# Kernel optimization log

Hardware: AMD Instinct MI355X
Metric: run time of the kernel (lower is better)

Reference implementation:

```python
import jax, jax.numpy as jnp
import numpy as np

EPS = 1e-5


def _layer_norm(x, w, b):
    mu = jnp.mean(x, axis=-1, keepdims=True)
    var = jnp.mean(jnp.square(x - mu), axis=-1, keepdims=True)
    return (x - mu) * jax.lax.rsqrt(var + EPS) * w + b


def setup_inputs() -> dict:
    key = jax.random.key(0)
    ks = jax.random.split(key, 6)
    B, S, N, CM, CZ, H = 1, 512, 512, 64, 128, 8
    return {
        "m_si": jax.random.normal(ks[0], (B, S, N, CM), jnp.float32),
        "z_ij": jax.random.normal(ks[1], (B, S, S, CZ), jnp.float32),
        "ln_m_w": jnp.ones((CM,), jnp.float32),
        "ln_m_b": jnp.zeros((CM,), jnp.float32),
        "ln_z_w": jnp.ones((CZ,), jnp.float32),
        "ln_z_b": jnp.zeros((CZ,), jnp.float32),
        "W_v": jax.random.normal(ks[2], (CM, CM), jnp.float32) / np.sqrt(CM),
        "W_b": jax.random.normal(ks[3], (H, CZ), jnp.float32) / np.sqrt(CZ),
        "W_g": jax.random.normal(ks[4], (CM, CM), jnp.float32) / np.sqrt(CM),
        "W_out": jax.random.normal(ks[5], (CM, CM), jnp.float32) / np.sqrt(CM),
    }


def reference(m_si, z_ij, ln_m_w, ln_m_b, ln_z_w, ln_z_b, W_v, W_b, W_g, W_out):
    H = W_b.shape[0]
    *lead, S, N, CM = m_si.shape
    D = CM // H  # head_dim

    m = _layer_norm(m_si, ln_m_w, ln_m_b)  # (..., s, n, c_m)

    # Pair bias logits -> softmax over j (second sequence axis)
    b = _layer_norm(z_ij, ln_z_w, ln_z_b) @ W_b.T          # (..., i, j, h)
    w = jax.nn.softmax(b, axis=-2)                          # softmax over j

    v = (m @ W_v.T).reshape(*lead, S, N, H, D)              # (..., j, n, h, d)
    g = jax.nn.sigmoid(m @ W_g.T).reshape(*lead, S, N, H, D)

    o = jnp.einsum("...ijh,...jnhd->...inhd", w, v)         # pair-weighted avg
    out = (g * o).reshape(*lead, S, N, CM) @ W_out.T
    return out
```

## Files before the change

kernel.cpp:

```cpp
#include <hip/hip_runtime.h>

typedef __bf16 bf16x8 __attribute__((ext_vector_type(8)));
typedef float  f32x4  __attribute__((ext_vector_type(4)));
typedef unsigned short u16x8 __attribute__((ext_vector_type(8)));

__device__ __forceinline__ float b2f(unsigned short u) {
    unsigned int x = ((unsigned int)u) << 16;
    float f; __builtin_memcpy(&f, &x, 4); return f;
}
__device__ __forceinline__ unsigned short f2b(float f) {
    unsigned int x; __builtin_memcpy(&x, &f, 4);
    unsigned int r = (x + 0x7FFFu + ((x >> 16) & 1u)) >> 16;
    return (unsigned short)r;
}
__device__ __forceinline__ void async16(void* lds, const void* g) {
    __builtin_amdgcn_global_load_lds((const __attribute__((address_space(1))) void*)g,
                                     (__attribute__((address_space(3))) void*)lds, 16, 0, 0);
}

__global__ __launch_bounds__(256) void k0_wcvt(
    const float* __restrict__ Wv, const float* __restrict__ Wg, unsigned short* __restrict__ Wp)
{
    const int idx = blockIdx.x * 256 + threadIdx.x;
    const int cg = idx >> 10, col = (idx >> 3) & 127, u = idx & 7;
    const int k = cg * 8 + u;
    const float v = (col < 64) ? Wv[col * 64 + k] : Wg[(col - 64) * 64 + k];
    Wp[idx] = f2b(v);
}

__global__ __launch_bounds__(256) void k1_ln_vg(
    const float* __restrict__ m, const float* __restrict__ lnw, const float* __restrict__ lnb,
    const unsigned short* __restrict__ Wp,
    unsigned short* __restrict__ vT, unsigned short* __restrict__ gB)
{
    __shared__ __align__(16) unsigned short Wl[8192];
    __shared__ __align__(16) unsigned short mhb[2048];
    __shared__ float vstage[32][65];
    __shared__ float gstage[32][65];
    const int t = threadIdx.x, w = t >> 6, lane = t & 63;
    const int n = blockIdx.x, s0 = blockIdx.y * 32;

#pragma unroll
    for (int r = 0; r < 4; r++)
        async16(&Wl[(r * 256 + t) * 8], Wp + (size_t)(r * 256 + t) * 8);

    const int rl = t >> 3, cg = t & 7, c8 = cg * 8;
    {
        const int s = s0 + rl;
        const float* src = &m[((size_t)s * 512 + n) * 64 + c8];
        float4 x0 = *(const float4*)src;
        float4 x1 = *(const float4*)(src + 4);
        float sum = x0.x+x0.y+x0.z+x0.w + x1.x+x1.y+x1.z+x1.w;
        float sq  = x0.x*x0.x+x0.y*x0.y+x0.z*x0.z+x0.w*x0.w
                  + x1.x*x1.x+x1.y*x1.y+x1.z*x1.z+x1.w*x1.w;
#pragma unroll
        for (int msk = 4; msk; msk >>= 1) { sum += __shfl_xor(sum, msk); sq += __shfl_xor(sq, msk); }
        float mu  = sum * (1.f / 64.f);
        float var = sq * (1.f / 64.f) - mu * mu;
        float rs  = rsqrtf(var + 1e-5f);
        float4 lw0 = *(const float4*)&lnw[c8], lw1 = *(const float4*)&lnw[c8 + 4];
        float4 lb0 = *(const float4*)&lnb[c8], lb1 = *(const float4*)&lnb[c8 + 4];
        u16x8 hb;
        hb[0] = f2b((x0.x - mu) * rs * lw0.x + lb0.x);
        hb[1] = f2b((x0.y - mu) * rs * lw0.y + lb0.y);
        hb[2] = f2b((x0.z - mu) * rs * lw0.z + lb0.z);
        hb[3] = f2b((x0.w - mu) * rs * lw0.w + lb0.w);
        hb[4] = f2b((x1.x - mu) * rs * lw1.x + lb1.x);
        hb[5] = f2b((x1.y - mu) * rs * lw1.y + lb1.y);
        hb[6] = f2b((x1.z - mu) * rs * lw1.z + lb1.z);
        hb[7] = f2b((x1.w - mu) * rs * lw1.w + lb1.w);
        *(u16x8*)&mhb[(cg * 32 + rl) * 8] = hb;
    }
    __syncthreads();

    const int quad = lane >> 4, lq = lane & 15;
    const int colbase = w * 32;
    f32x4 zero = {0.f, 0.f, 0.f, 0.f};
    f32x4 acc[2][2] = {{zero, zero}, {zero, zero}};
    bf16x8 af[2][2], bfr[2][2];
#pragma unroll
    for (int kk = 0; kk < 2; kk++) {
        const int ch = kk * 4 + quad;
#pragma unroll
        for (int mi = 0; mi < 2; mi++)
            af[mi][kk] = *(const bf16x8*)&mhb[(ch * 32 + mi * 16 + lq) * 8];
#pragma unroll
        for (int ni = 0; ni < 2; ni++)
            bfr[ni][kk] = *(const bf16x8*)&Wl[(ch * 128 + colbase + ni * 16 + lq) * 8];
    }
#pragma unroll
    for (int mi = 0; mi < 2; mi++)
#pragma unroll
        for (int ni = 0; ni < 2; ni++)
#pragma unroll
            for (int kk = 0; kk < 2; kk++)
                acc[mi][ni] = __builtin_amdgcn_mfma_f32_16x16x32_bf16(af[mi][kk], bfr[ni][kk], acc[mi][ni], 0, 0, 0);

    if (w < 2) {
#pragma unroll
        for (int mi = 0; mi < 2; mi++)
#pragma unroll
            for (int ni = 0; ni < 2; ni++)
#pragma unroll
                for (int rr = 0; rr < 4; rr++)
                    vstage[mi * 16 + quad * 4 + rr][colbase + ni * 16 + lq] = acc[mi][ni][rr];
    } else {
#pragma unroll
        for (int mi = 0; mi < 2; mi++)
#pragma unroll
            for (int ni = 0; ni < 2; ni++)
#pragma unroll
                for (int rr = 0; rr < 4; rr++) {
                    float gg = 1.f / (1.f + __expf(-acc[mi][ni][rr]));
                    gstage[mi * 16 + quad * 4 + rr][colbase - 64 + ni * 16 + lq] = gg;
                }
    }
    __syncthreads();

    {
        const int h = t >> 5, d = (t >> 2) & 7, jc = t & 3;
        u16x8 pk;
#pragma unroll
        for (int u = 0; u < 8; u++) pk[u] = f2b(vstage[jc * 8 + u][h * 8 + d]);
        size_t off = (size_t)h * 2097152 + (size_t)(n * 8 + d) * 512 + (size_t)(s0 + jc * 8);
        *(u16x8*)(vT + off) = pk;
    }
    {
        u16x8 gk;
#pragma unroll
        for (int u = 0; u < 8; u++) gk[u] = f2b(gstage[rl][c8 + u]);
        *(u16x8*)(gB + ((size_t)(s0 + rl) * 512 + n) * 64 + c8) = gk;
    }
}

__global__ __launch_bounds__(256) void k2_ln_b(
    const float* __restrict__ z, const float* __restrict__ lnw, const float* __restrict__ lnb,
    const float* __restrict__ Wb, float* __restrict__ bL)
{
    __shared__ float swb[1024];
    __shared__ float sw[128], sb[128];
    const int t = threadIdx.x;
    const int gtid = blockIdx.x * 256 + t;
    const int row = gtid >> 2, qt = gtid & 3;

    const float* src = z + (size_t)row * 128;
    float4 x[8];
#pragma unroll
    for (int q = 0; q < 8; q++)
        x[q] = *(const float4*)&src[q * 16 + qt * 4];

    *(float4*)&swb[t * 4] = *(const float4*)&Wb[t * 4];
    if (t < 32)      *(float4*)&sw[t * 4] = *(const float4*)&lnw[t * 4];
    else if (t < 64) *(float4*)&sb[(t - 32) * 4] = *(const float4*)&lnb[(t - 32) * 4];
    __syncthreads();

    float sum = 0.f, sq = 0.f;
#pragma unroll
    for (int q = 0; q < 8; q++) {
        sum += x[q].x + x[q].y + x[q].z + x[q].w;
        sq  += x[q].x*x[q].x + x[q].y*x[q].y + x[q].z*x[q].z + x[q].w*x[q].w;
    }
    sum += __shfl_xor(sum, 1); sq += __shfl_xor(sq, 1);
    sum += __shfl_xor(sum, 2); sq += __shfl_xor(sq, 2);
    const float mu  = sum * (1.f / 128.f);
    const float var = sq * (1.f / 128.f) - mu * mu;
    const float rs  = rsqrtf(var + 1e-5f);

    float acc[8];
#pragma unroll
    for (int h = 0; h < 8; h++) acc[h] = 0.f;
#pragma unroll
    for (int q = 0; q < 8; q++) {
        const int c0 = q * 16 + qt * 4;
        const float4 lw = *(const float4*)&sw[c0];
        const float4 lb = *(const float4*)&sb[c0];
        const float zn0 = (x[q].x - mu) * rs * lw.x + lb.x;
        const float zn1 = (x[q].y - mu) * rs * lw.y + lb.y;
        const float zn2 = (x[q].z - mu) * rs * lw.z + lb.z;
        const float zn3 = (x[q].w - mu) * rs * lw.w + lb.w;
#pragma unroll
        for (int h = 0; h < 8; h++) {
            const float4 wv = *(const float4*)&swb[h * 128 + c0];
            acc[h] += zn0 * wv.x + zn1 * wv.y + zn2 * wv.z + zn3 * wv.w;
        }
    }
#pragma unroll
    for (int h = 0; h < 8; h++) { acc[h] += __shfl_xor(acc[h], 1); acc[h] += __shfl_xor(acc[h], 2); }
    float2 o; o.x = acc[qt * 2]; o.y = acc[qt * 2 + 1];
    *(float2*)&bL[(size_t)row * 8 + qt * 2] = o;
}

__global__ __launch_bounds__(256) void k3_softmax(
    const float* __restrict__ bL, unsigned short* __restrict__ wp)
{
    __shared__ float bl[8][520];
    const int t = threadIdx.x;
    const int i = blockIdx.x;
    const float* src = bL + (size_t)i * 4096;
#pragma unroll
    for (int q = 0; q < 4; q++) {
        float4 a = *(const float4*)&src[q * 1024 + t * 4];
        int idx = q * 1024 + t * 4;
        bl[(idx+0)&7][(idx+0)>>3] = a.x;
        bl[(idx+1)&7][(idx+1)>>3] = a.y;
        bl[(idx+2)&7][(idx+2)>>3] = a.z;
        bl[(idx+3)&7][(idx+3)>>3] = a.w;
    }
    __syncthreads();
    const int h = t >> 5, l32 = t & 31;
    float vals[16];
    float mx = -1e30f;
#pragma unroll
    for (int jj = 0; jj < 16; jj++) { vals[jj] = bl[h][l32 + 32 * jj]; mx = fmaxf(mx, vals[jj]); }
#pragma unroll
    for (int msk = 1; msk < 32; msk <<= 1) mx = fmaxf(mx, __shfl_xor(mx, msk, 32));
    float s = 0.f;
#pragma unroll
    for (int jj = 0; jj < 16; jj++) { vals[jj] = __expf(vals[jj] - mx); s += vals[jj]; }
#pragma unroll
    for (int msk = 1; msk < 32; msk <<= 1) s += __shfl_xor(s, msk, 32);
    const float inv = 1.f / s;
    unsigned short* dst = wp + (size_t)h * 262144 + (size_t)i * 512;
#pragma unroll
    for (int jj = 0; jj < 16; jj++) dst[l32 + 32 * jj] = f2b(vals[jj] * inv);
}

__global__ __launch_bounds__(256) void k4_einsum(
    const unsigned short* __restrict__ wp, const unsigned short* __restrict__ vT,
    const unsigned short* __restrict__ gB, unsigned short* __restrict__ go)
{
    __shared__ __align__(16) unsigned short As[128 * 32];
    __shared__ __align__(16) unsigned short Bs[128 * 32];
    const int t = threadIdx.x;
    const int c0 = blockIdx.x * 128, i0 = blockIdx.y * 128, h = blockIdx.z;
    const unsigned short* Ab = wp + (size_t)h * 262144;
    const unsigned short* Bb = vT + (size_t)h * 2097152;
    const int w = t >> 6, lane = t & 63, quad = lane >> 4, lq = lane & 15;
    const int wi = w >> 1, wc = w & 1;

    f32x4 zero = {0.f, 0.f, 0.f, 0.f};
    f32x4 acc[4][4];
#pragma unroll
    for (int mi = 0; mi < 4; mi++)
#pragma unroll
        for (int ni = 0; ni < 4; ni++) acc[mi][ni] = zero;

    for (int k0 = 0; k0 < 512; k0 += 32) {
#pragma unroll
        for (int r = 0; r < 2; r++) {
            int idx = r * 256 + t;
            int row = idx >> 2, q = idx & 3;
            async16(&As[idx * 8], Ab + (size_t)(i0 + row) * 512 + k0 + q * 8);
            async16(&Bs[idx * 8], Bb + (size_t)(c0 + row) * 512 + k0 + q * 8);
        }
        __syncthreads();
        bf16x8 af[4], bfr[4];
#pragma unroll
        for (int mi = 0; mi < 4; mi++)
            af[mi] = *(const bf16x8*)&As[(wi * 64 + mi * 16 + lq) * 32 + quad * 8];
#pragma unroll
        for (int ni = 0; ni < 4; ni++)
            bfr[ni] = *(const bf16x8*)&Bs[(wc * 64 + ni * 16 + lq) * 32 + quad * 8];
#pragma unroll
        for (int mi = 0; mi < 4; mi++)
#pragma unroll
            for (int ni = 0; ni < 4; ni++)
                acc[mi][ni] = __builtin_amdgcn_mfma_f32_16x16x32_bf16(af[mi], bfr[ni], acc[mi][ni], 0, 0, 0);
        __syncthreads();
    }
#pragma unroll
    for (int mi = 0; mi < 4; mi++)
#pragma unroll
        for (int ni = 0; ni < 4; ni++)
#pragma unroll
            for (int rr = 0; rr < 4; rr++) {
                int ii = i0 + wi * 64 + mi * 16 + quad * 4 + rr;
                int c  = c0 + wc * 64 + ni * 16 + lq;
                size_t off = ((size_t)ii * 512 + (c >> 3)) * 64 + h * 8 + (c & 7);
                float gv = b2f(gB[off]);
                go[off] = f2b(acc[mi][ni][rr] * gv);
            }
}

__global__ __launch_bounds__(256) void k5_out(
    const unsigned short* __restrict__ go, const float* __restrict__ Wo, float* __restrict__ out)
{
    __shared__ __align__(16) unsigned short Bs[8192];
    const int t = threadIdx.x, w = t >> 6, lane = t & 63;
    const int quad = lane >> 4, lq = lane & 15;

    const int r0 = blockIdx.x * 64 + w * 16;
    const unsigned short* Ab = go + (size_t)r0 * 64;
    bf16x8 a[2];
#pragma unroll
    for (int kk = 0; kk < 2; kk++)
        a[kk] = *(const bf16x8*)&Ab[lq * 64 + (kk * 4 + quad) * 8];

#pragma unroll
    for (int r = 0; r < 2; r++) {
        const int idx = r * 256 + t;
        const int ch = idx >> 6, col = idx & 63;
        const float* srcw = &Wo[col * 64 + ch * 8];
        float4 w0 = *(const float4*)srcw;
        float4 w1 = *(const float4*)(srcw + 4);
        float v[8] = {w0.x, w0.y, w0.z, w0.w, w1.x, w1.y, w1.z, w1.w};
        u16x8 hi, lo;
#pragma unroll
        for (int u = 0; u < 8; u++) { hi[u] = f2b(v[u]); lo[u] = f2b(v[u] - b2f(hi[u])); }
        *(u16x8*)&Bs[(ch * 64 + col) * 8] = hi;
        *(u16x8*)&Bs[4096 + (ch * 64 + col) * 8] = lo;
    }
    __syncthreads();

    f32x4 zero = {0.f, 0.f, 0.f, 0.f};
#pragma unroll
    for (int ni = 0; ni < 4; ni++) {
        f32x4 acc = zero;
#pragma unroll
        for (int kk = 0; kk < 2; kk++) {
            const int ko = (kk * 4 + quad) * 64;
            bf16x8 bh = *(const bf16x8*)&Bs[(ko + ni * 16 + lq) * 8];
            bf16x8 bl = *(const bf16x8*)&Bs[4096 + (ko + ni * 16 + lq) * 8];
            acc = __builtin_amdgcn_mfma_f32_16x16x32_bf16(a[kk], bh, acc, 0, 0, 0);
            acc = __builtin_amdgcn_mfma_f32_16x16x32_bf16(a[kk], bl, acc, 0, 0, 0);
        }
#pragma unroll
        for (int rr = 0; rr < 4; rr++)
            out[(size_t)(r0 + quad * 4 + rr) * 64 + ni * 16 + lq] = acc[rr];
    }
}

extern "C" void kernel_launch(void* const* d_in, const int* in_sizes, int n_in,
                              void* d_out, int out_size, void* d_ws, size_t ws_size,
                              hipStream_t stream)
{
    (void)in_sizes; (void)n_in; (void)out_size; (void)ws_size;
    const float* m    = (const float*)d_in[0];
    const float* z    = (const float*)d_in[1];
    const float* lnmw = (const float*)d_in[2];
    const float* lnmb = (const float*)d_in[3];
    const float* lnzw = (const float*)d_in[4];
    const float* lnzb = (const float*)d_in[5];
    const float* Wv   = (const float*)d_in[6];
    const float* Wb   = (const float*)d_in[7];
    const float* Wg   = (const float*)d_in[8];
    const float* Wo   = (const float*)d_in[9];
    float* out = (float*)d_out;
    char* ws = (char*)d_ws;

    unsigned short* vT = (unsigned short*)(ws);
    unsigned short* wp = (unsigned short*)(ws + 33554432);
    unsigned short* gB = (unsigned short*)(ws + 37748736);
    float*          bL = (float*)(ws + 71303168);
    unsigned short* go = (unsigned short*)(ws + 79691776);
    unsigned short* Wp = wp;

    k0_wcvt   <<<dim3(32),      256, 0, stream>>>(Wv, Wg, Wp);
    k1_ln_vg  <<<dim3(512, 16), 256, 0, stream>>>(m, lnmw, lnmb, Wp, vT, gB);
    k2_ln_b   <<<dim3(4096),    256, 0, stream>>>(z, lnzw, lnzb, Wb, bL);
    k3_softmax<<<dim3(512),     256, 0, stream>>>(bL, wp);
    k4_einsum <<<dim3(32, 4, 8),256, 0, stream>>>(wp, vT, gB, go);
    k5_out    <<<dim3(4096),    256, 0, stream>>>(go, Wo, out);
}
```

Baseline: 369.0 us.

## Fuse pair-bias layernorm with softmax and coalesce gated einsum epilogue via LDS

Merges the z layernorm + bias projection kernel with the softmax kernel, so each block computes all 512 j logits for one row i in shared memory and drops the fp32 bL round-trip through global memory. The einsum epilogue now stages accumulators through an LDS tile and does 16-byte vectorized gate loads and output stores instead of scattered 2-byte accesses. The trade-off is that the fused kernel launches only 512 blocks, each doing 8 serial passes, which lowers parallelism for the z read. The epilogue also adds extra syncs and LDS traffic.

```diff
diff --git a/kernel.cpp b/kernel.cpp
--- a/kernel.cpp
+++ b/kernel.cpp
@@ -133,85 +133,73 @@
     }
 }
 
-__global__ __launch_bounds__(256) void k2_ln_b(
+__global__ __launch_bounds__(256) void k23_lnb_softmax(
     const float* __restrict__ z, const float* __restrict__ lnw, const float* __restrict__ lnb,
-    const float* __restrict__ Wb, float* __restrict__ bL)
+    const float* __restrict__ Wb, unsigned short* __restrict__ wp)
 {
     __shared__ float swb[1024];
     __shared__ float sw[128], sb[128];
+    __shared__ float sl[8 * 516];
     const int t = threadIdx.x;
-    const int gtid = blockIdx.x * 256 + t;
-    const int row = gtid >> 2, qt = gtid & 3;
-
-    const float* src = z + (size_t)row * 128;
-    float4 x[8];
-#pragma unroll
-    for (int q = 0; q < 8; q++)
-        x[q] = *(const float4*)&src[q * 16 + qt * 4];
+    const int i = blockIdx.x;
+    const int jt = t >> 2, qt = t & 3;
 
     *(float4*)&swb[t * 4] = *(const float4*)&Wb[t * 4];
     if (t < 32)      *(float4*)&sw[t * 4] = *(const float4*)&lnw[t * 4];
     else if (t < 64) *(float4*)&sb[(t - 32) * 4] = *(const float4*)&lnb[(t - 32) * 4];
     __syncthreads();
 
-    float sum = 0.f, sq = 0.f;
-#pragma unroll
-    for (int q = 0; q < 8; q++) {
-        sum += x[q].x + x[q].y + x[q].z + x[q].w;
-        sq  += x[q].x*x[q].x + x[q].y*x[q].y + x[q].z*x[q].z + x[q].w*x[q].w;
-    }
-    sum += __shfl_xor(sum, 1); sq += __shfl_xor(sq, 1);
-    sum += __shfl_xor(sum, 2); sq += __shfl_xor(sq, 2);
-    const float mu  = sum * (1.f / 128.f);
-    const float var = sq * (1.f / 128.f) - mu * mu;
-    const float rs  = rsqrtf(var + 1e-5f);
-
-    float acc[8];
-#pragma unroll
-    for (int h = 0; h < 8; h++) acc[h] = 0.f;
-#pragma unroll
-    for (int q = 0; q < 8; q++) {
-        const int c0 = q * 16 + qt * 4;
-        const float4 lw = *(const float4*)&sw[c0];
-        const float4 lb = *(const float4*)&sb[c0];
-        const float zn0 = (x[q].x - mu) * rs * lw.x + lb.x;
-        const float zn1 = (x[q].y - mu) * rs * lw.y + lb.y;
-        const float zn2 = (x[q].z - mu) * rs * lw.z + lb.z;
-        const float zn3 = (x[q].w - mu) * rs * lw.w + lb.w;
-#pragma unroll
-        for (int h = 0; h < 8; h++) {
-            const float4 wv = *(const float4*)&swb[h * 128 + c0];
-            acc[h] += zn0 * wv.x + zn1 * wv.y + zn2 * wv.z + zn3 * wv.w;
-        }
-    }
-#pragma unroll
-    for (int h = 0; h < 8; h++) { acc[h] += __shfl_xor(acc[h], 1); acc[h] += __shfl_xor(acc[h], 2); }
-    float2 o; o.x = acc[qt * 2]; o.y = acc[qt * 2 + 1];
-    *(float2*)&bL[(size_t)row * 8 + qt * 2] = o;
-}
-
-__global__ __launch_bounds__(256) void k3_softmax(
-    const float* __restrict__ bL, unsigned short* __restrict__ wp)
-{
-    __shared__ float bl[8][520];
-    const int t = threadIdx.x;
-    const int i = blockIdx.x;
-    const float* src = bL + (size_t)i * 4096;
-#pragma unroll
-    for (int q = 0; q < 4; q++) {
-        float4 a = *(const float4*)&src[q * 1024 + t * 4];
-        int idx = q * 1024 + t * 4;
-        bl[(idx+0)&7][(idx+0)>>3] = a.x;
-        bl[(idx+1)&7][(idx+1)>>3] = a.y;
-        bl[(idx+2)&7][(idx+2)>>3] = a.z;
-        bl[(idx+3)&7][(idx+3)>>3] = a.w;
-    }
-    __syncthreads();
+#pragma unroll 2
+    for (int pass = 0; pass < 8; pass++) {
+        const int j = pass * 64 + jt;
+        const float* src = z + ((size_t)i * 512 + j) * 128;
+        float4 x[8];
+#pragma unroll
+        for (int q = 0; q < 8; q++)
+            x[q] = *(const float4*)&src[q * 16 + qt * 4];
+
+        float sum = 0.f, sq = 0.f;
+#pragma unroll
+        for (int q = 0; q < 8; q++) {
+            sum += x[q].x + x[q].y + x[q].z + x[q].w;
+            sq  += x[q].x*x[q].x + x[q].y*x[q].y + x[q].z*x[q].z + x[q].w*x[q].w;
+        }
+        sum += __shfl_xor(sum, 1); sq += __shfl_xor(sq, 1);
+        sum += __shfl_xor(sum, 2); sq += __shfl_xor(sq, 2);
+        const float mu  = sum * (1.f / 128.f);
+        const float var = sq * (1.f / 128.f) - mu * mu;
+        const float rs  = rsqrtf(var + 1e-5f);
+
+        float acc[8];
+#pragma unroll
+        for (int h = 0; h < 8; h++) acc[h] = 0.f;
+#pragma unroll
+        for (int q = 0; q < 8; q++) {
+            const int c0 = q * 16 + qt * 4;
+            const float4 lw = *(const float4*)&sw[c0];
+            const float4 lb = *(const float4*)&sb[c0];
+            const float zn0 = (x[q].x - mu) * rs * lw.x + lb.x;
+            const float zn1 = (x[q].y - mu) * rs * lw.y + lb.y;
+            const float zn2 = (x[q].z - mu) * rs * lw.z + lb.z;
+            const float zn3 = (x[q].w - mu) * rs * lw.w + lb.w;
+#pragma unroll
+            for (int h = 0; h < 8; h++) {
+                const float4 wv = *(const float4*)&swb[h * 128 + c0];
+                acc[h] += zn0 * wv.x + zn1 * wv.y + zn2 * wv.z + zn3 * wv.w;
+            }
+        }
+#pragma unroll
+        for (int h = 0; h < 8; h++) { acc[h] += __shfl_xor(acc[h], 1); acc[h] += __shfl_xor(acc[h], 2); }
+        sl[(qt * 2)     * 516 + j] = acc[qt * 2];
+        sl[(qt * 2 + 1) * 516 + j] = acc[qt * 2 + 1];
+    }
+    __syncthreads();
+
     const int h = t >> 5, l32 = t & 31;
     float vals[16];
     float mx = -1e30f;
 #pragma unroll
-    for (int jj = 0; jj < 16; jj++) { vals[jj] = bl[h][l32 + 32 * jj]; mx = fmaxf(mx, vals[jj]); }
+    for (int jj = 0; jj < 16; jj++) { vals[jj] = sl[h * 516 + l32 + 32 * jj]; mx = fmaxf(mx, vals[jj]); }
 #pragma unroll
     for (int msk = 1; msk < 32; msk <<= 1) mx = fmaxf(mx, __shfl_xor(mx, msk, 32));
     float s = 0.f;
@@ -231,6 +219,7 @@
 {
     __shared__ __align__(16) unsigned short As[128 * 32];
     __shared__ __align__(16) unsigned short Bs[128 * 32];
+    __shared__ float cst[32][132];
     const int t = threadIdx.x;
     const int c0 = blockIdx.x * 128, i0 = blockIdx.y * 128, h = blockIdx.z;
     const unsigned short* Ab = wp + (size_t)h * 262144;
@@ -268,18 +257,39 @@
                 acc[mi][ni] = __builtin_amdgcn_mfma_f32_16x16x32_bf16(af[mi], bfr[ni], acc[mi][ni], 0, 0, 0);
         __syncthreads();
     }
-#pragma unroll
-    for (int mi = 0; mi < 4; mi++)
+
+    const int n0 = c0 >> 3;
+#pragma unroll
+    for (int mi = 0; mi < 4; mi++) {
 #pragma unroll
         for (int ni = 0; ni < 4; ni++)
 #pragma unroll
-            for (int rr = 0; rr < 4; rr++) {
-                int ii = i0 + wi * 64 + mi * 16 + quad * 4 + rr;
-                int c  = c0 + wc * 64 + ni * 16 + lq;
-                size_t off = ((size_t)ii * 512 + (c >> 3)) * 64 + h * 8 + (c & 7);
-                float gv = b2f(gB[off]);
-                go[off] = f2b(acc[mi][ni][rr] * gv);
-            }
+            for (int rr = 0; rr < 4; rr++)
+                cst[wi * 16 + quad * 4 + rr][wc * 64 + ni * 16 + lq] = acc[mi][ni][rr];
+        __syncthreads();
+#pragma unroll
+        for (int pp = 0; pp < 2; pp++) {
+            const int p = pp * 256 + t;
+            const int row = p >> 4, oct = p & 15;
+            const int ii = i0 + (row >> 4) * 64 + mi * 16 + (row & 15);
+            const int n  = n0 + oct;
+            const size_t off = ((size_t)ii * 512 + n) * 64 + h * 8;
+            const float4 a0 = *(const float4*)&cst[row][oct * 8];
+            const float4 a1 = *(const float4*)&cst[row][oct * 8 + 4];
+            const u16x8 gv = *(const u16x8*)(gB + off);
+            u16x8 ov;
+            ov[0] = f2b(a0.x * b2f(gv[0]));
+            ov[1] = f2b(a0.y * b2f(gv[1]));
+            ov[2] = f2b(a0.z * b2f(gv[2]));
+            ov[3] = f2b(a0.w * b2f(gv[3]));
+            ov[4] = f2b(a1.x * b2f(gv[4]));
+            ov[5] = f2b(a1.y * b2f(gv[5]));
+            ov[6] = f2b(a1.z * b2f(gv[6]));
+            ov[7] = f2b(a1.w * b2f(gv[7]));
+            *(u16x8*)(go + off) = ov;
+        }
+        __syncthreads();
+    }
 }
 
 __global__ __launch_bounds__(256) void k5_out(
@@ -351,14 +361,12 @@
     unsigned short* vT = (unsigned short*)(ws);
     unsigned short* wp = (unsigned short*)(ws + 33554432);
     unsigned short* gB = (unsigned short*)(ws + 37748736);
-    float*          bL = (float*)(ws + 71303168);
-    unsigned short* go = (unsigned short*)(ws + 79691776);
+    unsigned short* go = (unsigned short*)(ws + 71303168);
     unsigned short* Wp = wp;
 
-    k0_wcvt   <<<dim3(32),      256, 0, stream>>>(Wv, Wg, Wp);
-    k1_ln_vg  <<<dim3(512, 16), 256, 0, stream>>>(m, lnmw, lnmb, Wp, vT, gB);
-    k2_ln_b   <<<dim3(4096),    256, 0, stream>>>(z, lnzw, lnzb, Wb, bL);
-    k3_softmax<<<dim3(512),     256, 0, stream>>>(bL, wp);
-    k4_einsum <<<dim3(32, 4, 8),256, 0, stream>>>(wp, vT, gB, go);
-    k5_out    <<<dim3(4096),    256, 0, stream>>>(go, Wo, out);
-}
+    k0_wcvt        <<<dim3(32),       256, 0, stream>>>(Wv, Wg, Wp);
+    k1_ln_vg       <<<dim3(512, 16),  256, 0, stream>>>(m, lnmw, lnmb, Wp, vT, gB);
+    k23_lnb_softmax<<<dim3(512),      256, 0, stream>>>(z, lnzw, lnzb, Wb, wp);
+    k4_einsum      <<<dim3(32, 4, 8), 256, 0, stream>>>(wp, vT, gB, go);
+    k5_out         <<<dim3(4096),     256, 0, stream>>>(go, Wo, out);
+}
```

New measurement: 421.8 us. +14.3%, slower.
